# Kernel optimization log

Hardware: AMD Instinct MI355X
Metric: run time of the kernel (lower is better)

Reference implementation:

```python
import jax, jax.numpy as jnp
import numpy as np

ALPHA, GAMMA = 0.25, 2.0
THR = 0.85            # soft_target_threshold
KL_EPS = 1e-6
FOCAL_EPS = 1e-8
VOC = 96              # len(vocab); index VOC is blank/pad


def setup_inputs() -> dict:
    key = jax.random.key(0)
    ks = jax.random.split(key, 6)
    bs, nq, n_pts, num_gt, L = 16, 200, 25, 32, 25
    return {
        "pred_logits": jax.random.normal(ks[0], (bs, nq, n_pts, 1), jnp.float32),
        "pred_ctrl_points": jax.random.uniform(ks[1], (bs, nq, n_pts, 2), jnp.float32),
        "pred_text_logits": jax.random.normal(ks[2], (bs, nq, n_pts, VOC + 1), jnp.float32),
        "tgt_ctrl_points": jax.random.uniform(ks[3], (bs, num_gt, n_pts, 2), jnp.float32),
        "tgt_texts": jax.random.randint(ks[4], (bs, num_gt, L), 0, VOC + 1),
        "centroids": jax.random.normal(ks[5], (VOC, 256), jnp.float32),
    }


def _cost_matrix(pred_logits, pred_ctrl_points, pred_text_logits,
                 tgt_ctrl_points, tgt_texts, centroids):
    bs, nq, n_pts, _ = pred_logits.shape
    num_gt = tgt_texts.shape[1]

    # ---- focal classification cost (mean over control points) ----
    out_prob = jax.nn.sigmoid(pred_logits.reshape(bs * nq, n_pts, -1))
    neg = (1.0 - ALPHA) * out_prob ** GAMMA * (-jnp.log1p(-(out_prob - FOCAL_EPS)))
    neg = (1.0 - ALPHA) * out_prob ** GAMMA * (-jnp.log(1.0 - out_prob + FOCAL_EPS))
    pos = ALPHA * (1.0 - out_prob) ** GAMMA * (-jnp.log(out_prob + FOCAL_EPS))
    cost_class = (pos[..., 0] - neg[..., 0]).mean(-1, keepdims=True)  # [bs*nq, 1]

    # ---- L1 cdist over flattened control points ----
    out_pts = pred_ctrl_points.reshape(bs * nq, n_pts * 2)
    tgt_pts = tgt_ctrl_points.reshape(bs * num_gt, n_pts * 2)
    cost_kpts = jnp.abs(out_pts[:, None, :] - tgt_pts[None, :, :]).sum(-1)  # [bs*nq, bs*num_gt]

    # ---- linguistic KL-div cost (per-batch block diagonal) ----
    probs = jax.nn.softmax(pred_text_logits, axis=-1)          # [bs,nq,n_pts,VOC+1]
    pred_avg = probs[..., :VOC].mean(axis=2)                   # [bs,nq,VOC]
    P = pred_avg + KL_EPS
    P = P / P.sum(-1, keepdims=True)
    logP = jnp.log(P)

    # soft target distribution per character (generate_soft_target_sequence)
    cn = centroids / jnp.linalg.norm(centroids, axis=-1, keepdims=True)
    soft_all = THR * jnp.eye(VOC, dtype=P.dtype) + (1.0 - THR) * jax.nn.softmax(cn @ cn.T, axis=-1)  # [VOC,VOC]

    mask = (tgt_texts != VOC)                                  # [bs,num_gt,L]
    lengths = mask.sum(-1)                                     # [bs,num_gt]
    per_char = soft_all[jnp.clip(tgt_texts, 0, VOC - 1)]       # [bs,num_gt,L,VOC]
    tgt_avg = (per_char * mask[..., None]).sum(2) / jnp.maximum(lengths, 1)[..., None].astype(P.dtype)
    T = tgt_avg + KL_EPS
    T = T / T.sum(-1, keepdims=True)                           # [bs,num_gt,VOC]

    # KL(T || P) = sum T*logT - sum T*logP, vectorized over (query, gt)
    kl = (T * jnp.log(T)).sum(-1)[:, None, :] - jnp.einsum('bqv,bgv->bqg', logP, T)  # [bs,nq,num_gt]
    kl = jnp.where(lengths[:, None, :] == 0, 100.0, kl)

    # place per-batch blocks on the diagonal of the global cost matrix
    eye = jnp.eye(bs, dtype=kl.dtype)
    cost_text = jnp.einsum('bqg,bc->bqcg', kl, eye).reshape(bs * nq, bs * num_gt)

    C = 1.0 * cost_class + 1.0 * cost_kpts + 1.0 * cost_text   # class/coord/text weights = 1
    return C.reshape(bs, nq, bs * num_gt)


def reference(pred_logits, pred_ctrl_points, pred_text_logits,
              tgt_ctrl_points, tgt_texts, centroids):
    return _cost_matrix(pred_logits, pred_ctrl_points, pred_text_logits,
                        tgt_ctrl_points, tgt_texts, centroids)
```

## Files before the change

kernel.cpp:

```cpp
#include <hip/hip_runtime.h>
#include <hip/hip_bf16.h>

#define BS 16
#define NQ 200
#define NPTS 25
#define VOC 96
#define VOCP1 97
#define NGT 32
#define LSEQ 25
#define NCOL (BS*NGT)
#define NBQ (BS*NQ)
#define KL_EPS 1e-6f
#define FOCAL_EPS 1e-8f

__global__ __launch_bounds__(128) void kA(
        const float* __restrict__ pred_logits,
        const float* __restrict__ pred_text_logits,
        const float* __restrict__ centroids,
        float* __restrict__ logP,
        float* __restrict__ cost_class,
        float* __restrict__ soft)
{
    const int tid  = threadIdx.x;
    const int wave = tid >> 6, lane = tid & 63;
    __shared__ float s_buf[NPTS * VOCP1];
    __shared__ float s_invden[NPTS];
    __shared__ float s_part[2];

    if (blockIdx.x < NBQ) {
        const int bq = blockIdx.x;
        const float* tl = pred_text_logits + (size_t)bq * NPTS * VOCP1;
        for (int i = tid; i < NPTS * VOCP1; i += 128)
            s_buf[i] = __expf(tl[i]);
        __syncthreads();

        const int grp = tid >> 5, sub = tid & 31;
        for (int p0 = 0; p0 < NPTS; p0 += 4) {
            int p = p0 + grp;
            float s = 0.f;
            if (p < NPTS)
                for (int v = sub; v < VOCP1; v += 32) s += s_buf[p * VOCP1 + v];
            #pragma unroll
            for (int off = 16; off; off >>= 1) s += __shfl_xor(s, off, 32);
            if (p < NPTS && sub == 0) s_invden[p] = 1.0f / s;
        }

        if (wave == 0) {
            float cc = 0.f;
            if (lane < NPTS) {
                float x = pred_logits[bq * NPTS + lane];
                float p = 1.f / (1.f + __expf(-x));
                float pos = 0.25f * (1.f - p) * (1.f - p) * (-__logf(p + FOCAL_EPS));
                float neg = 0.75f * p * p * (-__logf(1.f - p + FOCAL_EPS));
                cc = pos - neg;
            }
            #pragma unroll
            for (int off = 32; off; off >>= 1) cc += __shfl_xor(cc, off);
            if (lane == 0) cost_class[bq] = cc * (1.0f / NPTS);
        }
        __syncthreads();

        float avg = 0.f;
        if (tid < VOC) {
            float a = 0.f;
            #pragma unroll
            for (int p = 0; p < NPTS; p++)
                a += s_buf[p * VOCP1 + tid] * s_invden[p];
            avg = a * (1.0f / NPTS);
        }
        float s = avg;
        #pragma unroll
        for (int off = 32; off; off >>= 1) s += __shfl_xor(s, off);
        if (lane == 0) s_part[wave] = s;
        __syncthreads();
        float denom = s_part[0] + s_part[1] + (float)VOC * KL_EPS;
        if (tid < VOC)
            logP[(size_t)bq * VOC + tid] = __logf((avg + KL_EPS) / denom);
    } else {
        const int i = blockIdx.x - NBQ;
        for (int k = tid; k < 64; k += 128)
            *(float4*)&s_buf[k * 4] = *(const float4*)&centroids[i * 256 + k * 4];
        __syncthreads();

        float e = 0.f;
        if (tid < VOC) {
            float dij = 0.f, djj = 0.f, dii = 0.f;
            const float4* cj = (const float4*)(centroids + (size_t)tid * 256);
            #pragma unroll 4
            for (int k = 0; k < 64; k++) {
                float4 b = cj[k];
                float4 a = *(const float4*)&s_buf[k * 4];
                dij += a.x * b.x + a.y * b.y + a.z * b.z + a.w * b.w;
                djj += b.x * b.x + b.y * b.y + b.z * b.z + b.w * b.w;
                dii += a.x * a.x + a.y * a.y + a.z * a.z + a.w * a.w;
            }
            float sim = dij * rsqrtf(dii * djj);
            e = __expf(sim);
        }
        float s = e;
        #pragma unroll
        for (int off = 32; off; off >>= 1) s += __shfl_xor(s, off);
        if (lane == 0) s_part[wave] = s;
        __syncthreads();
        float den = s_part[0] + s_part[1];
        if (tid < VOC) {
            float v = 0.15f * e / den;
            if (tid == i) v += 0.85f;
            soft[i * VOC + tid] = v;
        }
    }
}

__global__ __launch_bounds__(256) void kB(
        const int* __restrict__ tgt_texts,
        const float* __restrict__ soft,
        float* __restrict__ T,
        float* __restrict__ TlogT,
        int* __restrict__ lens)
{
    const int b   = blockIdx.x;
    const int tid = threadIdx.x;
    __shared__ float s_soft[VOC * VOC];
    __shared__ int   s_chars[NGT][LSEQ];

    for (int i = tid; i < VOC * VOC / 4; i += 256)
        ((float4*)s_soft)[i] = ((const float4*)soft)[i];
    for (int i = tid; i < NGT * LSEQ; i += 256)
        s_chars[i / LSEQ][i % LSEQ] = tgt_texts[b * NGT * LSEQ + i];
    __syncthreads();

    const int grp = tid >> 5, sub = tid & 31;
    for (int g = grp; g < NGT; g += 8) {
        int len = 0;
        float a0 = 0.f, a1 = 0.f, a2 = 0.f;
        for (int l = 0; l < LSEQ; l++) {
            int t = s_chars[g][l];
            if (t != VOC) {
                len++;
                const float* sr = s_soft + t * VOC;
                a0 += sr[sub]; a1 += sr[sub + 32]; a2 += sr[sub + 64];
            }
        }
        float inv = 1.f / (float)(len > 0 ? len : 1);
        a0 *= inv; a1 *= inv; a2 *= inv;
        float s = a0 + a1 + a2;
        #pragma unroll
        for (int off = 16; off; off >>= 1) s += __shfl_xor(s, off, 32);
        float denom = s + (float)VOC * KL_EPS;
        float t0 = (a0 + KL_EPS) / denom;
        float t1 = (a1 + KL_EPS) / denom;
        float t2 = (a2 + KL_EPS) / denom;
        const int bg = b * NGT + g;
        T[(size_t)bg * VOC + sub]      = t0;
        T[(size_t)bg * VOC + sub + 32] = t1;
        T[(size_t)bg * VOC + sub + 64] = t2;
        float tl = t0 * __logf(t0) + t1 * __logf(t1) + t2 * __logf(t2);
        #pragma unroll
        for (int off = 16; off; off >>= 1) tl += __shfl_xor(tl, off, 32);
        if (sub == 0) { TlogT[bg] = tl; lens[bg] = len; }
    }
}

#define TR 64
#define TC 64
__global__ __launch_bounds__(256) void kC(
        const float* __restrict__ pred_ctrl,
        const float* __restrict__ tgt_ctrl,
        const float* __restrict__ cost_class,
        float* __restrict__ out)
{
    const int r0  = (blockIdx.x >> 3) * TR;
    const int c0  = (blockIdx.x & 7) * TC;
    const int tid = threadIdx.x;
    const int tx  = tid & 15;
    const int ty  = tid >> 4;

    __shared__ float s_p[TR][52];
    __shared__ float s_t[TC][52];
    __shared__ float s_cc[TR];

    const float* pg = pred_ctrl + (size_t)r0 * 50;
    const float* tg = tgt_ctrl + (size_t)c0 * 50;
    for (int i = tid; i < TR * 50; i += 256) {
        int r = i / 50, d = i - r * 50;
        s_p[r][d] = pg[i];
        s_t[r][d] = tg[i];
    }
    if (tid < TR) s_cc[tid] = cost_class[r0 + tid];
    __syncthreads();

    float acc[4][4];
    #pragma unroll
    for (int i = 0; i < 4; i++)
        #pragma unroll
        for (int j = 0; j < 4; j++) acc[i][j] = 0.f;

    #pragma unroll
    for (int k = 0; k < 48; k += 4) {
        float4 p[4], t[4];
        #pragma unroll
        for (int i = 0; i < 4; i++) p[i] = *(const float4*)&s_p[ty * 4 + i][k];
        #pragma unroll
        for (int j = 0; j < 4; j++) t[j] = *(const float4*)&s_t[tx + 16 * j][k];
        #pragma unroll
        for (int i = 0; i < 4; i++)
            #pragma unroll
            for (int j = 0; j < 4; j++)
                acc[i][j] += fabsf(p[i].x - t[j].x) + fabsf(p[i].y - t[j].y)
                           + fabsf(p[i].z - t[j].z) + fabsf(p[i].w - t[j].w);
    }
    {
        float2 p[4], t[4];
        #pragma unroll
        for (int i = 0; i < 4; i++) p[i] = *(const float2*)&s_p[ty * 4 + i][48];
        #pragma unroll
        for (int j = 0; j < 4; j++) t[j] = *(const float2*)&s_t[tx + 16 * j][48];
        #pragma unroll
        for (int i = 0; i < 4; i++)
            #pragma unroll
            for (int j = 0; j < 4; j++)
                acc[i][j] += fabsf(p[i].x - t[j].x) + fabsf(p[i].y - t[j].y);
    }

    #pragma unroll
    for (int i = 0; i < 4; i++) {
        const int row = ty * 4 + i;
        const float cc = s_cc[row];
        #pragma unroll
        for (int j = 0; j < 4; j++)
            out[(size_t)(r0 + row) * NCOL + c0 + tx + 16 * j] = acc[i][j] + cc;
    }
}

__global__ __launch_bounds__(256) void kT(
        const float* __restrict__ logP,
        const float* __restrict__ T,
        const float* __restrict__ TlogT,
        const int* __restrict__ lens,
        float* __restrict__ out)
{
    const int r0  = blockIdx.x * 8;
    const int b   = r0 / NQ;
    const int tid = threadIdx.x;
    __shared__ float s_lp[8][VOC];
    __shared__ float s_Tt[VOC][NGT + 1];
    __shared__ float s_tl[NGT];
    __shared__ int   s_len[NGT];

    for (int i = tid; i < 8 * VOC; i += 256)
        s_lp[i / VOC][i % VOC] = logP[(size_t)r0 * VOC + i];
    for (int i = tid; i < NGT * VOC; i += 256) {
        int g = i / VOC, v = i - g * VOC;
        s_Tt[v][g] = T[(size_t)(b * NGT) * VOC + i];
    }
    if (tid < NGT) {
        s_tl[tid]  = TlogT[b * NGT + tid];
        s_len[tid] = lens[b * NGT + tid];
    }
    __syncthreads();

    const int g = tid & 31, rs = tid >> 5;
    float d = 0.f;
    #pragma unroll 8
    for (int v = 0; v < VOC; v++) d += s_lp[rs][v] * s_Tt[v][g];
    float val = (s_len[g] == 0) ? 100.f : (s_tl[g] - d);
    size_t o = (size_t)(r0 + rs) * NCOL + b * NGT + g;
    out[o] += val;
}

extern "C" void kernel_launch(void* const* d_in, const int* in_sizes, int n_in,
                              void* d_out, int out_size, void* d_ws, size_t ws_size,
                              hipStream_t stream) {
    const float* pred_logits = (const float*)d_in[0];
    const float* pred_ctrl   = (const float*)d_in[1];
    const float* pred_text   = (const float*)d_in[2];
    const float* tgt_ctrl    = (const float*)d_in[3];
    const int*   tgt_texts   = (const int*)d_in[4];
    const float* centroids   = (const float*)d_in[5];
    float* out = (float*)d_out;

    float* ws        = (float*)d_ws;
    float* logP      = ws;
    float* costclass = logP + (size_t)NBQ * VOC;
    float* soft      = costclass + NBQ;
    float* T         = soft + VOC * VOC;
    float* TlogT     = T + (size_t)NCOL * VOC;
    int*   lens      = (int*)(TlogT + NCOL);

    kA<<<NBQ + VOC, 128, 0, stream>>>(pred_logits, pred_text, centroids,
                                      logP, costclass, soft);
    kB<<<BS, 256, 0, stream>>>(tgt_texts, soft, T, TlogT, lens);
    kC<<<400, 256, 0, stream>>>(pred_ctrl, tgt_ctrl, costclass, out);
    kT<<<400, 256, 0, stream>>>(logP, T, TlogT, lens, out);
}
```

Before: 130.8 us.

## Fuse four kernels into two and recompute target distributions per block

Merges the logP, soft-target and cdist kernels into one launch of 256-thread blocks. The focal class cost is now computed inside the cdist blocks. The target-average kernel is folded into the KL kernel, so each of 400 blocks rebuilds T for its batch in shared memory instead of reading it from workspace. This removes two launches and the T/TlogT/lens round trips. In exchange, the T computation is redundantly repeated 25 times per batch and K2 uses a larger shared-memory footprint.

```diff
diff --git a/kernel.cpp b/kernel.cpp
--- a/kernel.cpp
+++ b/kernel.cpp
@@ -1,5 +1,4 @@
 #include <hip/hip_runtime.h>
-#include <hip/hip_bf16.h>
 
 #define BS 16
 #define NQ 200
@@ -13,50 +12,43 @@
 #define KL_EPS 1e-6f
 #define FOCAL_EPS 1e-8f
 
-__global__ __launch_bounds__(128) void kA(
+#define NB_LOGP NBQ
+#define NB_SOFT VOC
+#define NB_CDIST 400
+#define NB_K1 (NB_LOGP + NB_SOFT + NB_CDIST)
+
+__global__ __launch_bounds__(256) void K1(
         const float* __restrict__ pred_logits,
+        const float* __restrict__ pred_ctrl,
         const float* __restrict__ pred_text_logits,
+        const float* __restrict__ tgt_ctrl,
         const float* __restrict__ centroids,
         float* __restrict__ logP,
-        float* __restrict__ cost_class,
-        float* __restrict__ soft)
+        float* __restrict__ soft,
+        float* __restrict__ out)
 {
-    const int tid  = threadIdx.x;
-    const int wave = tid >> 6, lane = tid & 63;
-    __shared__ float s_buf[NPTS * VOCP1];
-    __shared__ float s_invden[NPTS];
-    __shared__ float s_part[2];
-
-    if (blockIdx.x < NBQ) {
-        const int bq = blockIdx.x;
+    __shared__ __align__(16) float smem[64 * 52 * 2 + 64];
+    const int tid = threadIdx.x;
+    const int bid = blockIdx.x;
+
+    if (bid < NB_LOGP) {
+        const int bq = bid;
+        float* s_buf    = smem;
+        float* s_invden = smem + 2432;
+        float* s_part   = smem + 2464;
+
         const float* tl = pred_text_logits + (size_t)bq * NPTS * VOCP1;
-        for (int i = tid; i < NPTS * VOCP1; i += 128)
+        for (int i = tid; i < NPTS * VOCP1; i += 256)
             s_buf[i] = __expf(tl[i]);
         __syncthreads();
 
         const int grp = tid >> 5, sub = tid & 31;
-        for (int p0 = 0; p0 < NPTS; p0 += 4) {
-            int p = p0 + grp;
+        for (int p = grp; p < NPTS; p += 8) {
             float s = 0.f;
-            if (p < NPTS)
-                for (int v = sub; v < VOCP1; v += 32) s += s_buf[p * VOCP1 + v];
+            for (int v = sub; v < VOCP1; v += 32) s += s_buf[p * VOCP1 + v];
             #pragma unroll
             for (int off = 16; off; off >>= 1) s += __shfl_xor(s, off, 32);
-            if (p < NPTS && sub == 0) s_invden[p] = 1.0f / s;
-        }
-
-        if (wave == 0) {
-            float cc = 0.f;
-            if (lane < NPTS) {
-                float x = pred_logits[bq * NPTS + lane];
-                float p = 1.f / (1.f + __expf(-x));
-                float pos = 0.25f * (1.f - p) * (1.f - p) * (-__logf(p + FOCAL_EPS));
-                float neg = 0.75f * p * p * (-__logf(1.f - p + FOCAL_EPS));
-                cc = pos - neg;
-            }
-            #pragma unroll
-            for (int off = 32; off; off >>= 1) cc += __shfl_xor(cc, off);
-            if (lane == 0) cost_class[bq] = cc * (1.0f / NPTS);
+            if (sub == 0) s_invden[p] = 1.0f / s;
         }
         __syncthreads();
 
@@ -71,15 +63,20 @@
         float s = avg;
         #pragma unroll
         for (int off = 32; off; off >>= 1) s += __shfl_xor(s, off);
+        const int wave = tid >> 6, lane = tid & 63;
         if (lane == 0) s_part[wave] = s;
         __syncthreads();
-        float denom = s_part[0] + s_part[1] + (float)VOC * KL_EPS;
+        float denom = s_part[0] + s_part[1] + s_part[2] + s_part[3]
+                    + (float)VOC * KL_EPS;
         if (tid < VOC)
             logP[(size_t)bq * VOC + tid] = __logf((avg + KL_EPS) / denom);
-    } else {
-        const int i = blockIdx.x - NBQ;
-        for (int k = tid; k < 64; k += 128)
-            *(float4*)&s_buf[k * 4] = *(const float4*)&centroids[i * 256 + k * 4];
+
+    } else if (bid < NB_LOGP + NB_SOFT) {
+        const int i = bid - NB_LOGP;
+        float4* s_c  = (float4*)smem;
+        float* s_part = smem + 256;
+        if (tid < 64)
+            s_c[tid] = ((const float4*)(centroids + (size_t)i * 256))[tid];
         __syncthreads();
 
         float e = 0.f;
@@ -89,7 +86,7 @@
             #pragma unroll 4
             for (int k = 0; k < 64; k++) {
                 float4 b = cj[k];
-                float4 a = *(const float4*)&s_buf[k * 4];
+                float4 a = s_c[k];
                 dij += a.x * b.x + a.y * b.y + a.z * b.z + a.w * b.w;
                 djj += b.x * b.x + b.y * b.y + b.z * b.z + b.w * b.w;
                 dii += a.x * a.x + a.y * a.y + a.z * a.z + a.w * a.w;
@@ -100,33 +97,115 @@
         float s = e;
         #pragma unroll
         for (int off = 32; off; off >>= 1) s += __shfl_xor(s, off);
+        const int wave = tid >> 6, lane = tid & 63;
         if (lane == 0) s_part[wave] = s;
         __syncthreads();
-        float den = s_part[0] + s_part[1];
+        float den = s_part[0] + s_part[1] + s_part[2] + s_part[3];
         if (tid < VOC) {
             float v = 0.15f * e / den;
             if (tid == i) v += 0.85f;
             soft[i * VOC + tid] = v;
         }
+
+    } else {
+        const int cid = bid - (NB_LOGP + NB_SOFT);
+        const int r0  = (cid >> 3) * 64;
+        const int c0  = (cid & 7) * 64;
+        float (*s_p)[52] = (float (*)[52])smem;
+        float (*s_t)[52] = (float (*)[52])(smem + 3328);
+        float* s_cc = smem + 6656;
+
+        const float* pg = pred_ctrl + (size_t)r0 * 50;
+        const float* tg = tgt_ctrl + (size_t)c0 * 50;
+        for (int i = tid; i < 64 * 50; i += 256) {
+            int r = i / 50, d = i - r * 50;
+            s_p[r][d] = pg[i];
+            s_t[r][d] = tg[i];
+        }
+        {
+            const int row4 = tid >> 2, q4 = tid & 3;
+            float cc = 0.f;
+            for (int p = q4; p < NPTS; p += 4) {
+                float x  = pred_logits[(size_t)(r0 + row4) * NPTS + p];
+                float pr = 1.f / (1.f + __expf(-x));
+                float pos = 0.25f * (1.f - pr) * (1.f - pr) * (-__logf(pr + FOCAL_EPS));
+                float neg = 0.75f * pr * pr * (-__logf(1.f - pr + FOCAL_EPS));
+                cc += pos - neg;
+            }
+            cc += __shfl_xor(cc, 1, 4);
+            cc += __shfl_xor(cc, 2, 4);
+            if (q4 == 0) s_cc[row4] = cc * (1.0f / NPTS);
+        }
+        __syncthreads();
+
+        const int tx = tid & 15;
+        const int ty = tid >> 4;
+        float acc[4][4];
+        #pragma unroll
+        for (int i = 0; i < 4; i++)
+            #pragma unroll
+            for (int j = 0; j < 4; j++) acc[i][j] = 0.f;
+
+        #pragma unroll
+        for (int k = 0; k < 48; k += 4) {
+            float4 p[4], t[4];
+            #pragma unroll
+            for (int i = 0; i < 4; i++) p[i] = *(const float4*)&s_p[ty * 4 + i][k];
+            #pragma unroll
+            for (int j = 0; j < 4; j++) t[j] = *(const float4*)&s_t[tx + 16 * j][k];
+            #pragma unroll
+            for (int i = 0; i < 4; i++)
+                #pragma unroll
+                for (int j = 0; j < 4; j++)
+                    acc[i][j] += fabsf(p[i].x - t[j].x) + fabsf(p[i].y - t[j].y)
+                               + fabsf(p[i].z - t[j].z) + fabsf(p[i].w - t[j].w);
+        }
+        {
+            float2 p[4], t[4];
+            #pragma unroll
+            for (int i = 0; i < 4; i++) p[i] = *(const float2*)&s_p[ty * 4 + i][48];
+            #pragma unroll
+            for (int j = 0; j < 4; j++) t[j] = *(const float2*)&s_t[tx + 16 * j][48];
+            #pragma unroll
+            for (int i = 0; i < 4; i++)
+                #pragma unroll
+                for (int j = 0; j < 4; j++)
+                    acc[i][j] += fabsf(p[i].x - t[j].x) + fabsf(p[i].y - t[j].y);
+        }
+
+        #pragma unroll
+        for (int i = 0; i < 4; i++) {
+            const int row = ty * 4 + i;
+            const float cc = s_cc[row];
+            #pragma unroll
+            for (int j = 0; j < 4; j++)
+                out[(size_t)(r0 + row) * NCOL + c0 + tx + 16 * j] = acc[i][j] + cc;
+        }
     }
 }
 
-__global__ __launch_bounds__(256) void kB(
+__global__ __launch_bounds__(256) void K2(
         const int* __restrict__ tgt_texts,
         const float* __restrict__ soft,
-        float* __restrict__ T,
-        float* __restrict__ TlogT,
-        int* __restrict__ lens)
+        const float* __restrict__ logP,
+        float* __restrict__ out)
 {
-    const int b   = blockIdx.x;
+    const int r0  = blockIdx.x * 8;
+    const int b   = r0 / NQ;
     const int tid = threadIdx.x;
     __shared__ float s_soft[VOC * VOC];
-    __shared__ int   s_chars[NGT][LSEQ];
+    __shared__ int   s_chars[NGT * LSEQ];
+    __shared__ float s_lp[8][VOC];
+    __shared__ float s_Tt[VOC][NGT + 1];
+    __shared__ float s_tl[NGT];
+    __shared__ int   s_len[NGT];
 
     for (int i = tid; i < VOC * VOC / 4; i += 256)
         ((float4*)s_soft)[i] = ((const float4*)soft)[i];
     for (int i = tid; i < NGT * LSEQ; i += 256)
-        s_chars[i / LSEQ][i % LSEQ] = tgt_texts[b * NGT * LSEQ + i];
+        s_chars[i] = tgt_texts[b * NGT * LSEQ + i];
+    for (int i = tid; i < 8 * VOC; i += 256)
+        s_lp[i / VOC][i % VOC] = logP[(size_t)r0 * VOC + i];
     __syncthreads();
 
     const int grp = tid >> 5, sub = tid & 31;
@@ -134,7 +213,7 @@
         int len = 0;
         float a0 = 0.f, a1 = 0.f, a2 = 0.f;
         for (int l = 0; l < LSEQ; l++) {
-            int t = s_chars[g][l];
+            int t = s_chars[g * LSEQ + l];
             if (t != VOC) {
                 len++;
                 const float* sr = s_soft + t * VOC;
@@ -150,112 +229,13 @@
         float t0 = (a0 + KL_EPS) / denom;
         float t1 = (a1 + KL_EPS) / denom;
         float t2 = (a2 + KL_EPS) / denom;
-        const int bg = b * NGT + g;
-        T[(size_t)bg * VOC + sub]      = t0;
-        T[(size_t)bg * VOC + sub + 32] = t1;
-        T[(size_t)bg * VOC + sub + 64] = t2;
+        s_Tt[sub][g]      = t0;
+        s_Tt[sub + 32][g] = t1;
+        s_Tt[sub + 64][g] = t2;
         float tl = t0 * __logf(t0) + t1 * __logf(t1) + t2 * __logf(t2);
         #pragma unroll
         for (int off = 16; off; off >>= 1) tl += __shfl_xor(tl, off, 32);
-        if (sub == 0) { TlogT[bg] = tl; lens[bg] = len; }
-    }
-}
-
-#define TR 64
-#define TC 64
-__global__ __launch_bounds__(256) void kC(
-        const float* __restrict__ pred_ctrl,
-        const float* __restrict__ tgt_ctrl,
-        const float* __restrict__ cost_class,
-        float* __restrict__ out)
-{
-    const int r0  = (blockIdx.x >> 3) * TR;
-    const int c0  = (blockIdx.x & 7) * TC;
-    const int tid = threadIdx.x;
-    const int tx  = tid & 15;
-    const int ty  = tid >> 4;
-
-    __shared__ float s_p[TR][52];
-    __shared__ float s_t[TC][52];
-    __shared__ float s_cc[TR];
-
-    const float* pg = pred_ctrl + (size_t)r0 * 50;
-    const float* tg = tgt_ctrl + (size_t)c0 * 50;
-    for (int i = tid; i < TR * 50; i += 256) {
-        int r = i / 50, d = i - r * 50;
-        s_p[r][d] = pg[i];
-        s_t[r][d] = tg[i];
-    }
-    if (tid < TR) s_cc[tid] = cost_class[r0 + tid];
-    __syncthreads();
-
-    float acc[4][4];
-    #pragma unroll
-    for (int i = 0; i < 4; i++)
-        #pragma unroll
-        for (int j = 0; j < 4; j++) acc[i][j] = 0.f;
-
-    #pragma unroll
-    for (int k = 0; k < 48; k += 4) {
-        float4 p[4], t[4];
-        #pragma unroll
-        for (int i = 0; i < 4; i++) p[i] = *(const float4*)&s_p[ty * 4 + i][k];
-        #pragma unroll
-        for (int j = 0; j < 4; j++) t[j] = *(const float4*)&s_t[tx + 16 * j][k];
-        #pragma unroll
-        for (int i = 0; i < 4; i++)
-            #pragma unroll
-            for (int j = 0; j < 4; j++)
-                acc[i][j] += fabsf(p[i].x - t[j].x) + fabsf(p[i].y - t[j].y)
-                           + fabsf(p[i].z - t[j].z) + fabsf(p[i].w - t[j].w);
-    }
-    {
-        float2 p[4], t[4];
-        #pragma unroll
-        for (int i = 0; i < 4; i++) p[i] = *(const float2*)&s_p[ty * 4 + i][48];
-        #pragma unroll
-        for (int j = 0; j < 4; j++) t[j] = *(const float2*)&s_t[tx + 16 * j][48];
-        #pragma unroll
-        for (int i = 0; i < 4; i++)
-            #pragma unroll
-            for (int j = 0; j < 4; j++)
-                acc[i][j] += fabsf(p[i].x - t[j].x) + fabsf(p[i].y - t[j].y);
-    }
-
-    #pragma unroll
-    for (int i = 0; i < 4; i++) {
-        const int row = ty * 4 + i;
-        const float cc = s_cc[row];
-        #pragma unroll
-        for (int j = 0; j < 4; j++)
-            out[(size_t)(r0 + row) * NCOL + c0 + tx + 16 * j] = acc[i][j] + cc;
-    }
-}
-
-__global__ __launch_bounds__(256) void kT(
-        const float* __restrict__ logP,
-        const float* __restrict__ T,
-        const float* __restrict__ TlogT,
-        const int* __restrict__ lens,
-        float* __restrict__ out)
-{
-    const int r0  = blockIdx.x * 8;
-    const int b   = r0 / NQ;
-    const int tid = threadIdx.x;
-    __shared__ float s_lp[8][VOC];
-    __shared__ float s_Tt[VOC][NGT + 1];
-    __shared__ float s_tl[NGT];
-    __shared__ int   s_len[NGT];
-
-    for (int i = tid; i < 8 * VOC; i += 256)
-        s_lp[i / VOC][i % VOC] = logP[(size_t)r0 * VOC + i];
-    for (int i = tid; i < NGT * VOC; i += 256) {
-        int g = i / VOC, v = i - g * VOC;
-        s_Tt[v][g] = T[(size_t)(b * NGT) * VOC + i];
-    }
-    if (tid < NGT) {
-        s_tl[tid]  = TlogT[b * NGT + tid];
-        s_len[tid] = lens[b * NGT + tid];
+        if (sub == 0) { s_tl[g] = tl; s_len[g] = len; }
     }
     __syncthreads();
 
@@ -279,17 +259,11 @@
     const float* centroids   = (const float*)d_in[5];
     float* out = (float*)d_out;
 
-    float* ws        = (float*)d_ws;
-    float* logP      = ws;
-    float* costclass = logP + (size_t)NBQ * VOC;
-    float* soft      = costclass + NBQ;
-    float* T         = soft + VOC * VOC;
-    float* TlogT     = T + (size_t)NCOL * VOC;
-    int*   lens      = (int*)(TlogT + NCOL);
-
-    kA<<<NBQ + VOC, 128, 0, stream>>>(pred_logits, pred_text, centroids,
-                                      logP, costclass, soft);
-    kB<<<BS, 256, 0, stream>>>(tgt_texts, soft, T, TlogT, lens);
-    kC<<<400, 256, 0, stream>>>(pred_ctrl, tgt_ctrl, costclass, out);
-    kT<<<400, 256, 0, stream>>>(logP, T, TlogT, lens, out);
+    float* ws   = (float*)d_ws;
+    float* logP = ws;
+    float* soft = logP + (size_t)NBQ * VOC;
+
+    K1<<<NB_K1, 256, 0, stream>>>(pred_logits, pred_ctrl, pred_text,
+                                  tgt_ctrl, centroids, logP, soft, out);
+    K2<<<400, 256, 0, stream>>>(tgt_texts, soft, logP, out);
 }
```

New measurement: 126.0 us. 1.04x faster.
